# Kernel tuning notes

Measured on AMD Instinct MI355X. Metric: run time of the kernel, lower is better.

The kernel has to match this reference:

```python
import jax, jax.numpy as jnp
import numpy as np

NUM_HEADS = 16
HEAD_SIZE = 64
N_EMBED = 1024
BLOCK_SIZE = 1024
BATCH = 8


def setup_inputs() -> dict:
    key = jax.random.key(0)
    ks = jax.random.split(key, 8)
    s_in = 1.0 / np.sqrt(N_EMBED)
    x = jax.random.normal(ks[0], (BATCH, BLOCK_SIZE, N_EMBED), dtype=jnp.float32)
    Wq = jax.random.normal(ks[1], (N_EMBED, N_EMBED), dtype=jnp.float32) * s_in
    Wk = jax.random.normal(ks[2], (N_EMBED, N_EMBED), dtype=jnp.float32) * s_in
    Wv = jax.random.normal(ks[3], (N_EMBED, N_EMBED), dtype=jnp.float32) * s_in
    Wo = jax.random.normal(ks[4], (N_EMBED, N_EMBED), dtype=jnp.float32) * s_in
    bo = jnp.zeros((N_EMBED,), dtype=jnp.float32)
    W1 = jax.random.normal(ks[5], (N_EMBED, N_EMBED), dtype=jnp.float32) * s_in
    b1 = jnp.zeros((N_EMBED,), dtype=jnp.float32)
    return {"x": x, "Wq": Wq, "Wk": Wk, "Wv": Wv, "Wo": Wo, "bo": bo, "W1": W1, "b1": b1}


def reference(x, Wq, Wk, Wv, Wo, bo, W1, b1):
    B, T, E = x.shape
    H, Dh = NUM_HEADS, HEAD_SIZE
    # per-head projections (bias=False), concatenated weights reshaped to heads
    q = (x @ Wq).reshape(B, T, H, Dh)
    k = (x @ Wk).reshape(B, T, H, Dh)
    v = (x @ Wv).reshape(B, T, H, Dh)
    scale = Dh ** -0.5
    scores = jnp.einsum("bqhd,bkhd->bhqk", q, k) * scale  # [B,H,T,T]
    causal = jnp.tril(jnp.ones((T, T), dtype=bool))
    scores = jnp.where(causal, scores, jnp.float32(-jnp.inf))
    attn = jax.nn.softmax(scores, axis=-1)
    out = jnp.einsum("bhqk,bkhd->bqhd", attn, v).reshape(B, T, E)
    out = out @ Wo + bo  # output projection
    # FeedForward: Linear(E, E) + ReLU
    out = jax.nn.relu(out @ W1 + b1)
    return out
```

## Files before the change

### kernel.cpp

```cpp
#include <hip/hip_runtime.h>

typedef __bf16 bf16x8 __attribute__((ext_vector_type(8)));
typedef float f32x4 __attribute__((ext_vector_type(4)));
typedef short short4v __attribute__((ext_vector_type(4)));
typedef short short8v __attribute__((ext_vector_type(8)));

#define DEVI static __device__ __forceinline__

DEVI short f2bf(float f) {
    union { __bf16 b; short s; } u;
    u.b = (__bf16)f;
    return u.s;
}

DEVI void gld16(const void* g, void* l) {
    __builtin_amdgcn_global_load_lds(
        (const __attribute__((address_space(1))) unsigned int*)g,
        (__attribute__((address_space(3))) unsigned int*)l, 16, 0, 0);
}

__global__ __launch_bounds__(256) void cvt_x_kernel(const float* __restrict__ x,
                                                    short* __restrict__ xb) {
    int i = (blockIdx.x * 256 + threadIdx.x) * 8;
    f32x4 a = *(const f32x4*)(x + i);
    f32x4 b = *(const f32x4*)(x + i + 4);
    short8v o;
    o[0]=f2bf(a[0]); o[1]=f2bf(a[1]); o[2]=f2bf(a[2]); o[3]=f2bf(a[3]);
    o[4]=f2bf(b[0]); o[5]=f2bf(b[1]); o[6]=f2bf(b[2]); o[7]=f2bf(b[3]);
    *(short8v*)(xb + i) = o;
}

__global__ __launch_bounds__(256) void wtrans5_kernel(const float* __restrict__ w0,
                                                      const float* __restrict__ w1,
                                                      const float* __restrict__ w2,
                                                      const float* __restrict__ w3,
                                                      const float* __restrict__ w4,
                                                      short* __restrict__ dst) {
    const float* w;
    switch (blockIdx.z) {
        case 0: w = w0; break;
        case 1: w = w1; break;
        case 2: w = w2; break;
        case 3: w = w3; break;
        default: w = w4; break;
    }
    short* wt = dst + (size_t)blockIdx.z * 1048576;
    __shared__ float t[64][68];
    const int tid = threadIdx.x;
    const int k0 = blockIdx.x * 64, n0 = blockIdx.y * 64;
#pragma unroll
    for (int it = 0; it < 4; ++it) {
        int r = (tid >> 4) + it * 16;
        int cc = (tid & 15) * 4;
        f32x4 vv = *(const f32x4*)(w + (k0 + r) * 1024 + n0 + cc);
        *(f32x4*)&t[r][cc] = vv;
    }
    __syncthreads();
    if (blockIdx.z == 3) {
#pragma unroll
        for (int it = 0; it < 4; ++it) {
            int r = (tid >> 4) + it * 16;
            int cc = (tid & 15) * 4;
            short4v o;
            o[0] = f2bf(t[r][cc + 0]);
            o[1] = f2bf(t[r][cc + 1]);
            o[2] = f2bf(t[r][cc + 2]);
            o[3] = f2bf(t[r][cc + 3]);
            *(short4v*)(wt + (k0 + r) * 1024 + n0 + cc) = o;
        }
    } else {
#pragma unroll
        for (int it = 0; it < 4; ++it) {
            int n = (tid >> 4) + it * 16;
            int kc = (tid & 15) * 4;
            short4v o;
            o[0] = f2bf(t[kc + 0][n]);
            o[1] = f2bf(t[kc + 1][n]);
            o[2] = f2bf(t[kc + 2][n]);
            o[3] = f2bf(t[kc + 3][n]);
            *(short4v*)(wt + (n0 + n) * 1024 + k0 + kc) = o;
        }
    }
}

__global__ __launch_bounds__(256) void bcomb_kernel(const float* __restrict__ bo,
                                                    const float* __restrict__ W1,
                                                    const float* __restrict__ b1,
                                                    float* __restrict__ out) {
    __shared__ f32x4 red[64][4];
    const int tid = threadIdx.x;
    const int jg = tid >> 2;
    const int nq = tid & 3;
    const int n = blockIdx.x * 16 + nq * 4;
    f32x4 acc = {0.f, 0.f, 0.f, 0.f};
#pragma unroll 4
    for (int jj = 0; jj < 16; ++jj) {
        int j = jg * 16 + jj;
        float s = bo[j];
        f32x4 w = *(const f32x4*)(W1 + j * 1024 + n);
        acc[0] += s * w[0]; acc[1] += s * w[1]; acc[2] += s * w[2]; acc[3] += s * w[3];
    }
    red[jg][nq] = acc;
    __syncthreads();
#pragma unroll
    for (int s = 32; s >= 1; s >>= 1) {
        if (jg < s) {
            f32x4 a = red[jg][nq], b2 = red[jg + s][nq];
            a[0] += b2[0]; a[1] += b2[1]; a[2] += b2[2]; a[3] += b2[3];
            red[jg][nq] = a;
        }
        __syncthreads();
    }
    if (jg == 0) {
        f32x4 r = red[0][nq];
        f32x4 bb = *(const f32x4*)(b1 + n);
        r[0] += bb[0]; r[1] += bb[1]; r[2] += bb[2]; r[3] += bb[3];
        *(f32x4*)(out + n) = r;
    }
}

__global__ __launch_bounds__(256, 2) void gemm64_bt(const short* __restrict__ A,
                                                    const short* __restrict__ Bt,
                                                    short* __restrict__ outp) {
    __shared__ short As[64 * 64];
    __shared__ short Bs[64 * 64];
    const int tid = threadIdx.x;
    const int lane = tid & 63;
    const int wid = tid >> 6;
    const int g = lane >> 4, c = lane & 15;
    const int wr = wid >> 1, wc = wid & 1;
    const int m0 = blockIdx.x * 64, n0 = blockIdx.y * 64;

    const f32x4 fz = {0.f, 0.f, 0.f, 0.f};
    f32x4 acc[2][2];
#pragma unroll
    for (int m = 0; m < 2; ++m)
#pragma unroll
        for (int n = 0; n < 2; ++n) acc[m][n] = fz;

    for (int kt = 0; kt < 16; ++kt) {
        const int k0 = kt * 64;
        __syncthreads();
#pragma unroll
        for (int st = 0; st < 2; ++st) {
            int ci = st * 256 + tid;
            int r = ci >> 3;
            int cc = ((ci & 7) ^ (r & 7)) << 3;
            gld16(A + (m0 + r) * 1024 + k0 + cc, (char*)As + ci * 16);
            gld16(Bt + (n0 + r) * 1024 + k0 + cc, (char*)Bs + ci * 16);
        }
        __syncthreads();
#pragma unroll
        for (int kk = 0; kk < 2; ++kk) {
            bf16x8 af[2], bfr[2];
#pragma unroll
            for (int m = 0; m < 2; ++m) {
                int row = wr * 32 + m * 16 + c;
                af[m] = *(const bf16x8*)((const char*)As + row * 128 + ((kk * 64 + g * 16) ^ ((row & 7) << 4)));
            }
#pragma unroll
            for (int n = 0; n < 2; ++n) {
                int row = wc * 32 + n * 16 + c;
                bfr[n] = *(const bf16x8*)((const char*)Bs + row * 128 + ((kk * 64 + g * 16) ^ ((row & 7) << 4)));
            }
#pragma unroll
            for (int m = 0; m < 2; ++m)
#pragma unroll
                for (int n = 0; n < 2; ++n)
                    acc[m][n] = __builtin_amdgcn_mfma_f32_16x16x32_bf16(af[m], bfr[n], acc[m][n], 0, 0, 0);
        }
    }

#pragma unroll
    for (int n = 0; n < 2; ++n) {
        const int col = n0 + wc * 32 + n * 16 + c;
#pragma unroll
        for (int m = 0; m < 2; ++m) {
            const int row0 = m0 + wr * 32 + m * 16 + g * 4;
#pragma unroll
            for (int i = 0; i < 4; ++i)
                outp[(row0 + i) * 1024 + col] = f2bf(acc[m][n][i]);
        }
    }
}

template<int MODE>
__global__ __launch_bounds__(256, 2) void gemm_bt(const short* __restrict__ A,
                                                  const short* __restrict__ Bt,
                                                  const float* __restrict__ bias,
                                                  void* __restrict__ outp) {
    __shared__ short As[128 * 64];
    __shared__ short Bs[128 * 64];
    const int tid = threadIdx.x;
    const int lane = tid & 63;
    const int wid = tid >> 6;
    const int g = lane >> 4, c = lane & 15;
    const int wr = wid >> 1, wc = wid & 1;
    const int m0 = blockIdx.x * 128, n0 = blockIdx.y * 128;

    const f32x4 fz = {0.f, 0.f, 0.f, 0.f};
    f32x4 acc[4][4];
#pragma unroll
    for (int m = 0; m < 4; ++m)
#pragma unroll
        for (int n = 0; n < 4; ++n) acc[m][n] = fz;

    for (int kt = 0; kt < 16; ++kt) {
        const int k0 = kt * 64;
        __syncthreads();
#pragma unroll
        for (int st = 0; st < 4; ++st) {
            int ci = st * 256 + tid;
            int r = ci >> 3;
            int cc = ((ci & 7) ^ (r & 7)) << 3;
            gld16(A + (m0 + r) * 1024 + k0 + cc, (char*)As + ci * 16);
            gld16(Bt + (n0 + r) * 1024 + k0 + cc, (char*)Bs + ci * 16);
        }
        __syncthreads();
#pragma unroll
        for (int kk = 0; kk < 2; ++kk) {
            bf16x8 af[4], bfr[4];
#pragma unroll
            for (int m = 0; m < 4; ++m) {
                int row = wr * 64 + m * 16 + c;
                af[m] = *(const bf16x8*)((const char*)As + row * 128 + ((kk * 64 + g * 16) ^ ((row & 7) << 4)));
            }
#pragma unroll
            for (int n = 0; n < 4; ++n) {
                int row = wc * 64 + n * 16 + c;
                bfr[n] = *(const bf16x8*)((const char*)Bs + row * 128 + ((kk * 64 + g * 16) ^ ((row & 7) << 4)));
            }
#pragma unroll
            for (int m = 0; m < 4; ++m)
#pragma unroll
                for (int n = 0; n < 4; ++n)
                    acc[m][n] = __builtin_amdgcn_mfma_f32_16x16x32_bf16(af[m], bfr[n], acc[m][n], 0, 0, 0);
        }
    }

#pragma unroll
    for (int n = 0; n < 4; ++n) {
        const int col = n0 + wc * 64 + n * 16 + c;
        float bv = 0.f;
        if (MODE == 2) bv = bias[col];
#pragma unroll
        for (int m = 0; m < 4; ++m) {
            const int row0 = m0 + wr * 64 + m * 16 + g * 4;
#pragma unroll
            for (int i = 0; i < 4; ++i) {
                const int row = row0 + i;
                float val = acc[m][n][i];
                if (MODE == 0) {
                    short* qkv = (short*)outp;
                    int which = col >> 10;
                    int hc = col & 1023;
                    if (which == 0) val *= 0.18033688011112042f;
                    int dst = which * 8388608 +
                              (((row >> 10) * 16 + (hc >> 6)) * 1024 + (row & 1023)) * 64 + (hc & 63);
                    qkv[dst] = f2bf(val);
                } else {
                    ((float*)outp)[row * 1024 + col] = fmaxf(val + bv, 0.f);
                }
            }
        }
    }
}

__global__ __launch_bounds__(256, 2) void attn_kernel(const short* __restrict__ qp,
                                                      const short* __restrict__ kp,
                                                      const short* __restrict__ vp,
                                                      short* __restrict__ ao) {
    __shared__ short Ks[64 * 64];
    __shared__ short Vt[64 * 64];
    __shared__ short Ps[4][32 * 64];
    const int tid = threadIdx.x;
    const int lane = tid & 63;
    const int wid = tid >> 6;
    const int g = lane >> 4, c = lane & 15;
    const int bh = blockIdx.y;
    const int base = bh * 65536;
    const int b = bh >> 4, h = bh & 15;

    const int r0 = tid >> 3, c0 = (tid & 7) << 3;
    const int vt0 = (tid >> 4) * 4;
    const int vd0 = (tid & 15) * 4;

    const f32x4 fz = {0.f, 0.f, 0.f, 0.f};

    bf16x8 kreg0, kreg1;
    short4v vreg0, vreg1, vreg2, vreg3;

#pragma unroll 1
    for (int ph = 0; ph < 2; ++ph) {
        const int qt = ph ? (7 - blockIdx.x) : blockIdx.x;
        const int q0 = qt * 128;
        const int nkt = (qt + 1) * 2;
        const int qlo = q0 + wid * 32;

        bf16x8 qf[2][2];
#pragma unroll
        for (int m = 0; m < 2; ++m)
#pragma unroll
            for (int hh = 0; hh < 2; ++hh)
                qf[m][hh] = *(const bf16x8*)(qp + base + (qlo + m * 16 + c) * 64 + hh * 32 + g * 8);

        f32x4 accO[2][4];
#pragma unroll
        for (int m = 0; m < 2; ++m)
#pragma unroll
            for (int n = 0; n < 4; ++n) accO[m][n] = fz;
        float mrow[2][4], lsum[2][4];
#pragma unroll
        for (int m = 0; m < 2; ++m)
#pragma unroll
            for (int i = 0; i < 4; ++i) { mrow[m][i] = -1e30f; lsum[m][i] = 0.f; }

        kreg0 = *(const bf16x8*)(kp + base + r0 * 64 + c0);
        kreg1 = *(const bf16x8*)(kp + base + (r0 + 32) * 64 + c0);
        vreg0 = *(const short4v*)(vp + base + (vt0 + 0) * 64 + vd0);
        vreg1 = *(const short4v*)(vp + base + (vt0 + 1) * 64 + vd0);
        vreg2 = *(const short4v*)(vp + base + (vt0 + 2) * 64 + vd0);
        vreg3 = *(const short4v*)(vp + base + (vt0 + 3) * 64 + vd0);

        for (int kt = 0; kt < nkt; ++kt) {
            __syncthreads();
            *(bf16x8*)((char*)Ks + r0 * 128 + ((c0 * 2) ^ ((r0 & 7) << 4))) = kreg0;
            *(bf16x8*)((char*)Ks + (r0 + 32) * 128 + ((c0 * 2) ^ ((r0 & 7) << 4))) = kreg1;
#pragma unroll
            for (int i = 0; i < 4; ++i) {
                short4v w; w[0] = vreg0[i]; w[1] = vreg1[i]; w[2] = vreg2[i]; w[3] = vreg3[i];
                int d = vd0 + i;
                *(short4v*)((char*)Vt + d * 128 + ((vt0 * 2) ^ ((d & 7) << 4))) = w;
            }
            if (kt + 1 < nkt) {
                const short* kp2 = kp + base + (kt + 1) * 4096;
                const short* vp2 = vp + base + (kt + 1) * 4096;
                kreg0 = *(const bf16x8*)(kp2 + r0 * 64 + c0);
                kreg1 = *(const bf16x8*)(kp2 + (r0 + 32) * 64 + c0);
                vreg0 = *(const short4v*)(vp2 + (vt0 + 0) * 64 + vd0);
                vreg1 = *(const short4v*)(vp2 + (vt0 + 1) * 64 + vd0);
                vreg2 = *(const short4v*)(vp2 + (vt0 + 2) * 64 + vd0);
                vreg3 = *(const short4v*)(vp2 + (vt0 + 3) * 64 + vd0);
            }
            __syncthreads();

            const int klo = kt * 64;
            const bool skip = klo > qlo + 31;
            if (!skip) {
                const bool needMask = (klo + 63 > qlo);
                int nlim = 4;
                if (needMask) {
                    nlim = ((qlo + 31 - klo) >> 4) + 1;
                    if (nlim > 4) nlim = 4;
                }

                f32x4 s[2][4];
#pragma unroll
                for (int m = 0; m < 2; ++m)
#pragma unroll
                    for (int n = 0; n < 4; ++n) s[m][n] = fz;
                __builtin_amdgcn_s_setprio(1);
#pragma unroll
                for (int n = 0; n < 4; ++n) {
                    if (n < nlim) {
                        int row = n * 16 + c;
                        int swz = (c & 7) << 4;
                        bf16x8 kf0 = *(const bf16x8*)((const char*)Ks + row * 128 + ((g * 16) ^ swz));
                        bf16x8 kf1 = *(const bf16x8*)((const char*)Ks + row * 128 + ((64 + g * 16) ^ swz));
#pragma unroll
                        for (int m = 0; m < 2; ++m) {
                            s[m][n] = __builtin_amdgcn_mfma_f32_16x16x32_bf16(qf[m][0], kf0, s[m][n], 0, 0, 0);
                            s[m][n] = __builtin_amdgcn_mfma_f32_16x16x32_bf16(qf[m][1], kf1, s[m][n], 0, 0, 0);
                        }
                    }
                }
                __builtin_amdgcn_s_setprio(0);

                float pm[2][4];
#pragma unroll
                for (int m = 0; m < 2; ++m)
#pragma unroll
                    for (int i = 0; i < 4; ++i) pm[m][i] = -1e30f;
                if (needMask) {
#pragma unroll
                    for (int n = 0; n < 4; ++n) {
                        int kg = klo + n * 16 + c;
#pragma unroll
                        for (int m = 0; m < 2; ++m)
#pragma unroll
                            for (int i = 0; i < 4; ++i) {
                                float vv = s[m][n][i];
                                vv = (kg <= qlo + m * 16 + g * 4 + i) ? vv : -1e30f;
                                s[m][n][i] = vv;
                                pm[m][i] = fmaxf(pm[m][i], vv);
                            }
                    }
                } else {
#pragma unroll
                    for (int n = 0; n < 4; ++n)
#pragma unroll
                        for (int m = 0; m < 2; ++m)
#pragma unroll
                            for (int i = 0; i < 4; ++i)
                                pm[m][i] = fmaxf(pm[m][i], s[m][n][i]);
                }
#pragma unroll
                for (int off = 1; off < 16; off <<= 1)
#pragma unroll
                    for (int m = 0; m < 2; ++m)
#pragma unroll
                        for (int i = 0; i < 4; ++i)
                            pm[m][i] = fmaxf(pm[m][i], __shfl_xor(pm[m][i], off));

                int need = 0;
#pragma unroll
                for (int m = 0; m < 2; ++m)
#pragma unroll
                    for (int i = 0; i < 4; ++i)
                        need |= (pm[m][i] > mrow[m][i] + 8.f) ? 1 : 0;
                if (__any(need)) {
#pragma unroll
                    for (int m = 0; m < 2; ++m)
#pragma unroll
                        for (int i = 0; i < 4; ++i) {
                            float mnew = fmaxf(mrow[m][i], pm[m][i]);
                            float corr = exp2f(mrow[m][i] - mnew);
                            mrow[m][i] = mnew;
                            lsum[m][i] *= corr;
#pragma unroll
                            for (int n = 0; n < 4; ++n) accO[m][n][i] *= corr;
                        }
                }
#pragma unroll
                for (int m = 0; m < 2; ++m)
#pragma unroll
                    for (int n = 0; n < 4; ++n)
#pragma unroll
                        for (int i = 0; i < 4; ++i) {
                            float pv = exp2f(s[m][n][i] - mrow[m][i]);
                            s[m][n][i] = pv;
                            lsum[m][i] += pv;
                        }

                asm volatile("s_waitcnt lgkmcnt(0)" ::: "memory");
                __builtin_amdgcn_sched_barrier(0);
#pragma unroll
                for (int m = 0; m < 2; ++m)
#pragma unroll
                    for (int n = 0; n < 4; ++n) {
                        int t = n * 16 + c;
#pragma unroll
                        for (int i = 0; i < 4; ++i) {
                            int q = m * 16 + g * 4 + i;
                            *(short*)((char*)&Ps[wid][0] + q * 128 + ((t * 2) ^ ((q & 7) << 4))) =
                                f2bf(s[m][n][i]);
                        }
                    }
                asm volatile("s_waitcnt lgkmcnt(0)" ::: "memory");
                __builtin_amdgcn_sched_barrier(0);

#pragma unroll
                for (int kk = 0; kk < 2; ++kk) {
                    bf16x8 paf[2];
#pragma unroll
                    for (int m = 0; m < 2; ++m)
                        paf[m] = *(const bf16x8*)((const char*)&Ps[wid][0] +
                                                  (m * 16 + c) * 128 + ((kk * 64 + g * 16) ^ ((c & 7) << 4)));
                    __builtin_amdgcn_s_setprio(1);
#pragma unroll
                    for (int n = 0; n < 4; ++n) {
                        int d = n * 16 + c;
                        bf16x8 vf = *(const bf16x8*)((const char*)Vt + d * 128 +
                                                     ((kk * 64 + g * 16) ^ ((d & 7) << 4)));
#pragma unroll
                        for (int m = 0; m < 2; ++m)
                            accO[m][n] = __builtin_amdgcn_mfma_f32_16x16x32_bf16(paf[m], vf, accO[m][n], 0, 0, 0);
                    }
                    __builtin_amdgcn_s_setprio(0);
                }
            }
        }

#pragma unroll
        for (int m = 0; m < 2; ++m) {
            float lrow[4];
#pragma unroll
            for (int i = 0; i < 4; ++i) lrow[i] = lsum[m][i];
#pragma unroll
            for (int off = 1; off < 16; off <<= 1)
#pragma unroll
                for (int i = 0; i < 4; ++i)
                    lrow[i] += __shfl_xor(lrow[i], off);
            float inv[4];
#pragma unroll
            for (int i = 0; i < 4; ++i) inv[i] = __builtin_amdgcn_rcpf(lrow[i]);
#pragma unroll
            for (int n = 0; n < 4; ++n)
#pragma unroll
                for (int i = 0; i < 4; ++i) {
                    int t = qlo + m * 16 + g * 4 + i;
                    float o = accO[m][n][i] * inv[i];
                    ao[(b * 1024 + t) * 1024 + h * 64 + n * 16 + c] = f2bf(o);
                }
        }
    }
}

extern "C" void kernel_launch(void* const* d_in, const int* in_sizes, int n_in,
                              void* d_out, int out_size, void* d_ws, size_t ws_size,
                              hipStream_t stream) {
    const float* x  = (const float*)d_in[0];
    const float* Wq = (const float*)d_in[1];
    const float* Wk = (const float*)d_in[2];
    const float* Wv = (const float*)d_in[3];
    const float* Wo = (const float*)d_in[4];
    const float* bo = (const float*)d_in[5];
    const float* W1 = (const float*)d_in[6];
    const float* b1 = (const float*)d_in[7];

    char* ws = (char*)d_ws;
    short* xb    = (short*)(ws + 0);
    short* wallT = (short*)(ws + 16777216);
    short* qb    = (short*)(ws + 27262976);
    short* kb    = qb + 8388608;
    short* vb    = qb + 16777216;
    short* ao    = xb;
    short* wqkvT = wallT;
    short* woBF  = wallT + 3145728;
    short* w1T   = wallT + 4194304;
    short* wcombT= wqkvT;
    float* bcomb = (float*)(ws + 16777216 + 2097152);

    cvt_x_kernel<<<4096, 256, 0, stream>>>(x, xb);
    wtrans5_kernel<<<dim3(16, 16, 5), 256, 0, stream>>>(Wq, Wk, Wv, Wo, W1, wallT);

    gemm_bt<0><<<dim3(64, 24), 256, 0, stream>>>(xb, wqkvT, nullptr, (void*)qb);
    gemm64_bt<<<dim3(16, 16), 256, 0, stream>>>(w1T, woBF, wcombT);
    bcomb_kernel<<<64, 256, 0, stream>>>(bo, W1, b1, bcomb);
    attn_kernel<<<dim3(4, 128), 256, 0, stream>>>(qb, kb, vb, ao);
    gemm_bt<2><<<dim3(64, 8), 256, 0, stream>>>(ao, wcombT, bcomb, d_out);
}
```

Baseline: 172.6 us.

## Split attention KV loop across two wave groups and merge softmax partials

The attention block grows from 256 to 512 threads. Two groups of four waves each take alternate 64-key tiles for the same query rows and hold separate K/V LDS buffers. At the end, group 1 writes its partial output, running max and running sum to LDS, and group 0 merges the two online-softmax states before writing. This halves the serial KV iteration count per query tile to expose more parallelism, at the cost of extra LDS, the merge step, and higher per-block resource use.

```diff
diff --git a/kernel.cpp b/kernel.cpp
--- a/kernel.cpp
+++ b/kernel.cpp
@@ -266,24 +266,29 @@
     }
 }
 
-__global__ __launch_bounds__(256, 2) void attn_kernel(const short* __restrict__ qp,
+__global__ __launch_bounds__(512, 2) void attn_kernel(const short* __restrict__ qp,
                                                       const short* __restrict__ kp,
                                                       const short* __restrict__ vp,
                                                       short* __restrict__ ao) {
-    __shared__ short Ks[64 * 64];
-    __shared__ short Vt[64 * 64];
-    __shared__ short Ps[4][32 * 64];
+    __shared__ short LDSS[32768];
     const int tid = threadIdx.x;
     const int lane = tid & 63;
     const int wid = tid >> 6;
+    const int grp = wid >> 2;
+    const int lwid = wid & 3;
+    const int gtid = tid & 255;
     const int g = lane >> 4, c = lane & 15;
     const int bh = blockIdx.y;
     const int base = bh * 65536;
     const int b = bh >> 4, h = bh & 15;
 
-    const int r0 = tid >> 3, c0 = (tid & 7) << 3;
-    const int vt0 = (tid >> 4) * 4;
-    const int vd0 = (tid & 15) * 4;
+    short* Ksb = LDSS + grp * 4096;
+    short* Vtb = LDSS + 8192 + grp * 4096;
+    short* Psb = LDSS + 16384 + wid * 2048;
+
+    const int r0 = gtid >> 3, c0 = (gtid & 7) << 3;
+    const int vt0 = (gtid >> 4) * 4;
+    const int vd0 = (gtid & 15) * 4;
 
     const f32x4 fz = {0.f, 0.f, 0.f, 0.f};
 
@@ -294,8 +299,8 @@
     for (int ph = 0; ph < 2; ++ph) {
         const int qt = ph ? (7 - blockIdx.x) : blockIdx.x;
         const int q0 = qt * 128;
-        const int nkt = (qt + 1) * 2;
-        const int qlo = q0 + wid * 32;
+        const int qlo = q0 + lwid * 32;
+        const int nt = qt + 1;
 
         bf16x8 qf[2][2];
 #pragma unroll
@@ -315,26 +320,32 @@
 #pragma unroll
             for (int i = 0; i < 4; ++i) { mrow[m][i] = -1e30f; lsum[m][i] = 0.f; }
 
-        kreg0 = *(const bf16x8*)(kp + base + r0 * 64 + c0);
-        kreg1 = *(const bf16x8*)(kp + base + (r0 + 32) * 64 + c0);
-        vreg0 = *(const short4v*)(vp + base + (vt0 + 0) * 64 + vd0);
-        vreg1 = *(const short4v*)(vp + base + (vt0 + 1) * 64 + vd0);
-        vreg2 = *(const short4v*)(vp + base + (vt0 + 2) * 64 + vd0);
-        vreg3 = *(const short4v*)(vp + base + (vt0 + 3) * 64 + vd0);
-
-        for (int kt = 0; kt < nkt; ++kt) {
+        {
+            const short* kp2 = kp + base + grp * 4096;
+            const short* vp2 = vp + base + grp * 4096;
+            kreg0 = *(const bf16x8*)(kp2 + r0 * 64 + c0);
+            kreg1 = *(const bf16x8*)(kp2 + (r0 + 32) * 64 + c0);
+            vreg0 = *(const short4v*)(vp2 + (vt0 + 0) * 64 + vd0);
+            vreg1 = *(const short4v*)(vp2 + (vt0 + 1) * 64 + vd0);
+            vreg2 = *(const short4v*)(vp2 + (vt0 + 2) * 64 + vd0);
+            vreg3 = *(const short4v*)(vp2 + (vt0 + 3) * 64 + vd0);
+        }
+
+        for (int it = 0; it < nt; ++it) {
+            const int kt = grp + 2 * it;
             __syncthreads();
-            *(bf16x8*)((char*)Ks + r0 * 128 + ((c0 * 2) ^ ((r0 & 7) << 4))) = kreg0;
-            *(bf16x8*)((char*)Ks + (r0 + 32) * 128 + ((c0 * 2) ^ ((r0 & 7) << 4))) = kreg1;
+            *(bf16x8*)((char*)Ksb + r0 * 128 + ((c0 * 2) ^ ((r0 & 7) << 4))) = kreg0;
+            *(bf16x8*)((char*)Ksb + (r0 + 32) * 128 + ((c0 * 2) ^ ((r0 & 7) << 4))) = kreg1;
 #pragma unroll
             for (int i = 0; i < 4; ++i) {
                 short4v w; w[0] = vreg0[i]; w[1] = vreg1[i]; w[2] = vreg2[i]; w[3] = vreg3[i];
                 int d = vd0 + i;
-                *(short4v*)((char*)Vt + d * 128 + ((vt0 * 2) ^ ((d & 7) << 4))) = w;
-            }
-            if (kt + 1 < nkt) {
-                const short* kp2 = kp + base + (kt + 1) * 4096;
-                const short* vp2 = vp + base + (kt + 1) * 4096;
+                *(short4v*)((char*)Vtb + d * 128 + ((vt0 * 2) ^ ((d & 7) << 4))) = w;
+            }
+            if (it + 1 < nt) {
+                const int ktn = grp + 2 * (it + 1);
+                const short* kp2 = kp + base + ktn * 4096;
+                const short* vp2 = vp + base + ktn * 4096;
                 kreg0 = *(const bf16x8*)(kp2 + r0 * 64 + c0);
                 kreg1 = *(const bf16x8*)(kp2 + (r0 + 32) * 64 + c0);
                 vreg0 = *(const short4v*)(vp2 + (vt0 + 0) * 64 + vd0);
@@ -345,7 +356,7 @@
             __syncthreads();
 
             const int klo = kt * 64;
-            const bool skip = klo > qlo + 31;
+            const bool skip = (klo > qlo + 31);
             if (!skip) {
                 const bool needMask = (klo + 63 > qlo);
                 int nlim = 4;
@@ -365,8 +376,8 @@
                     if (n < nlim) {
                         int row = n * 16 + c;
                         int swz = (c & 7) << 4;
-                        bf16x8 kf0 = *(const bf16x8*)((const char*)Ks + row * 128 + ((g * 16) ^ swz));
-                        bf16x8 kf1 = *(const bf16x8*)((const char*)Ks + row * 128 + ((64 + g * 16) ^ swz));
+                        bf16x8 kf0 = *(const bf16x8*)((const char*)Ksb + row * 128 + ((g * 16) ^ swz));
+                        bf16x8 kf1 = *(const bf16x8*)((const char*)Ksb + row * 128 + ((64 + g * 16) ^ swz));
 #pragma unroll
                         for (int m = 0; m < 2; ++m) {
                             s[m][n] = __builtin_amdgcn_mfma_f32_16x16x32_bf16(qf[m][0], kf0, s[m][n], 0, 0, 0);
@@ -452,7 +463,7 @@
 #pragma unroll
                         for (int i = 0; i < 4; ++i) {
                             int q = m * 16 + g * 4 + i;
-                            *(short*)((char*)&Ps[wid][0] + q * 128 + ((t * 2) ^ ((q & 7) << 4))) =
+                            *(short*)((char*)Psb + q * 128 + ((t * 2) ^ ((q & 7) << 4))) =
                                 f2bf(s[m][n][i]);
                         }
                     }
@@ -464,13 +475,13 @@
                     bf16x8 paf[2];
 #pragma unroll
                     for (int m = 0; m < 2; ++m)
-                        paf[m] = *(const bf16x8*)((const char*)&Ps[wid][0] +
+                        paf[m] = *(const bf16x8*)((const char*)Psb +
                                                   (m * 16 + c) * 128 + ((kk * 64 + g * 16) ^ ((c & 7) << 4)));
                     __builtin_amdgcn_s_setprio(1);
 #pragma unroll
                     for (int n = 0; n < 4; ++n) {
                         int d = n * 16 + c;
-                        bf16x8 vf = *(const bf16x8*)((const char*)Vt + d * 128 +
+                        bf16x8 vf = *(const bf16x8*)((const char*)Vtb + d * 128 +
                                                      ((kk * 64 + g * 16) ^ ((d & 7) << 4)));
 #pragma unroll
                         for (int m = 0; m < 2; ++m)
@@ -481,27 +492,62 @@
             }
         }
 
+        float lrow[2][4];
 #pragma unroll
         for (int m = 0; m < 2; ++m) {
-            float lrow[4];
-#pragma unroll
-            for (int i = 0; i < 4; ++i) lrow[i] = lsum[m][i];
+#pragma unroll
+            for (int i = 0; i < 4; ++i) lrow[m][i] = lsum[m][i];
 #pragma unroll
             for (int off = 1; off < 16; off <<= 1)
 #pragma unroll
                 for (int i = 0; i < 4; ++i)
-                    lrow[i] += __shfl_xor(lrow[i], off);
-            float inv[4];
-#pragma unroll
-            for (int i = 0; i < 4; ++i) inv[i] = __builtin_amdgcn_rcpf(lrow[i]);
-#pragma unroll
-            for (int n = 0; n < 4; ++n)
+                    lrow[m][i] += __shfl_xor(lrow[m][i], off);
+        }
+
+        __syncthreads();
+        float* slot = (float*)((char*)LDSS + lwid * 16384) + lane * 48;
+        if (grp == 1) {
+#pragma unroll
+            for (int m = 0; m < 2; ++m)
+#pragma unroll
+                for (int n = 0; n < 4; ++n)
+                    *(f32x4*)(slot + (m * 4 + n) * 4) = accO[m][n];
+#pragma unroll
+            for (int m = 0; m < 2; ++m)
 #pragma unroll
                 for (int i = 0; i < 4; ++i) {
-                    int t = qlo + m * 16 + g * 4 + i;
-                    float o = accO[m][n][i] * inv[i];
-                    ao[(b * 1024 + t) * 1024 + h * 64 + n * 16 + c] = f2bf(o);
-                }
+                    slot[32 + m * 4 + i] = mrow[m][i];
+                    slot[40 + m * 4 + i] = lrow[m][i];
+                }
+        }
+        __syncthreads();
+        if (grp == 0) {
+#pragma unroll
+            for (int m = 0; m < 2; ++m) {
+                float mb[4], lb[4], sa[4], sb[4];
+#pragma unroll
+                for (int i = 0; i < 4; ++i) {
+                    mb[i] = slot[32 + m * 4 + i];
+                    lb[i] = slot[40 + m * 4 + i];
+                    float ms = fmaxf(mrow[m][i], mb[i]);
+                    sa[i] = exp2f(mrow[m][i] - ms);
+                    sb[i] = exp2f(mb[i] - ms);
+                }
+                float inv[4];
+#pragma unroll
+                for (int i = 0; i < 4; ++i)
+                    inv[i] = __builtin_amdgcn_rcpf(lrow[m][i] * sa[i] + lb[i] * sb[i]);
+#pragma unroll
+                for (int n = 0; n < 4; ++n) {
+                    f32x4 ob = *(const f32x4*)(slot + (m * 4 + n) * 4);
+#pragma unroll
+                    for (int i = 0; i < 4; ++i) {
+                        int t = qlo + m * 16 + g * 4 + i;
+                        float o = (accO[m][n][i] * sa[i] + ob[i] * sb[i]) * inv[i];
+                        ao[(b * 1024 + t) * 1024 + h * 64 + n * 16 + c] = f2bf(o);
+                    }
+                }
+            }
         }
     }
 }
@@ -537,6 +583,6 @@
     gemm_bt<0><<<dim3(64, 24), 256, 0, stream>>>(xb, wqkvT, nullptr, (void*)qb);
     gemm64_bt<<<dim3(16, 16), 256, 0, stream>>>(w1T, woBF, wcombT);
     bcomb_kernel<<<64, 256, 0, stream>>>(bo, W1, b1, bcomb);
-    attn_kernel<<<dim3(4, 128), 256, 0, stream>>>(qb, kb, vb, ao);
+    attn_kernel<<<dim3(4, 128), 512, 0, stream>>>(qb, kb, vb, ao);
     gemm_bt<2><<<dim3(64, 8), 256, 0, stream>>>(ao, wcombT, bcomb, d_out);
 }
```

Result: slower. 183.1 us (+6.1%).
